# Kernel tuning notes

Hardware: AMD Instinct MI355X
Metric: run time of the kernel (lower is better)

The kernel has to match this reference:

```python
import jax, jax.numpy as jnp
import numpy as np

N = 50000      # nodes per graph
G = 5          # num_graphs
F = 128        # in_channels
E0 = 800000    # random edges (avg degree 16)
H1, C1 = 8, 8  # conv1: heads=8, out=8 -> concat 64
C2 = 16        # conv2: heads=1, out=out_channels
NEG_SLOPE = 0.2


def setup_inputs() -> dict:
    key = jax.random.key(0)
    ks = jax.random.split(key, 12)
    x = jax.random.normal(ks[0], (G, N, F), dtype=jnp.float32)
    er = jax.random.randint(ks[1], (G, 2, E0), 0, N, dtype=jnp.int32)
    loops = jnp.broadcast_to(jnp.arange(N, dtype=jnp.int32), (G, 2, N))
    edge_index = jnp.concatenate([er, loops], axis=-1)  # [G, 2, E0+N] with self loops
    s = 0.1
    W1 = jax.random.normal(ks[2], (F, H1 * C1), jnp.float32) * s
    a_src1 = jax.random.normal(ks[3], (H1, C1), jnp.float32) * s
    a_dst1 = jax.random.normal(ks[4], (H1, C1), jnp.float32) * s
    b1 = jnp.zeros((H1 * C1,), jnp.float32)
    W2 = jax.random.normal(ks[5], (H1 * C1, C2), jnp.float32) * s
    a_src2 = jax.random.normal(ks[6], (1, C2), jnp.float32) * s
    a_dst2 = jax.random.normal(ks[7], (1, C2), jnp.float32) * s
    b2 = jnp.zeros((C2,), jnp.float32)
    Wf = jax.random.normal(ks[8], (C2 * G, 2), jnp.float32) * s
    bf = jnp.zeros((2,), jnp.float32)
    return {"x": x, "edge_index": edge_index, "W1": W1, "a_src1": a_src1,
            "a_dst1": a_dst1, "b1": b1, "W2": W2, "a_src2": a_src2,
            "a_dst2": a_dst2, "b2": b2, "Wf": Wf, "bf": bf}


def gat_layer(x, src, dst, W, a_src, a_dst, b):
    # x: [N, Fin]; src/dst: [E]; W: [Fin, H*C]; a_src/a_dst: [H, C]; b: [H*C]
    H, C = a_src.shape
    h = (x @ W).reshape(-1, H, C)                       # [N, H, C]
    alpha_s = jnp.einsum('nhc,hc->nh', h, a_src)        # [N, H]
    alpha_d = jnp.einsum('nhc,hc->nh', h, a_dst)
    e = jax.nn.leaky_relu(alpha_s[src] + alpha_d[dst], NEG_SLOPE)  # [E, H]
    m = jax.ops.segment_max(e, dst, num_segments=N)     # per-target softmax (stable)
    ex = jnp.exp(e - m[dst])
    denom = jax.ops.segment_sum(ex, dst, num_segments=N)
    alpha = ex / (denom[dst] + 1e-16)                   # [E, H]
    out = jax.ops.segment_sum(alpha[:, :, None] * h[src], dst, num_segments=N)  # [N, H, C]
    return out.reshape(-1, H * C) + b


def reference(x, edge_index, W1, a_src1, a_dst1, b1, W2, a_src2, a_dst2, b2, Wf, bf):
    def per_graph(xg, eg):
        src, dst = eg[0], eg[1]  # messages flow source -> target (PyG convention)
        h = jax.nn.relu(gat_layer(xg, src, dst, W1, a_src1, a_dst1, b1))
        return gat_layer(h, src, dst, W2, a_src2, a_dst2, b2)  # [N, C2]
    x_seq = jax.vmap(per_graph)(x, edge_index)          # [G, N, C2]
    x_seq = jnp.transpose(x_seq, (1, 0, 2)).reshape(N, G * C2)
    return x_seq @ Wf + bf                               # [N, 2]
```

## Files before the change

### kernel.cpp

```cpp
#include <hip/hip_runtime.h>

constexpr int N_NODES = 50000;
constexpr int G = 5;
constexpr int E = 850000;
constexpr int GN = G * N_NODES;
constexpr int GE = G * E;
constexpr float SLOPE = 0.2f;

constexpr int NPB = 1024;
constexpr int NBUK = (GN + NPB - 1) / NPB;
constexpr int EPB = 4096;
constexpr int NBLK_E = (GE + EPB - 1) / EPB;

static __device__ __forceinline__ float lrelu(float e) {
    return e > 0.f ? e : SLOPE * e;
}
static __device__ __forceinline__ unsigned short f2h(float f) {
    union { _Float16 h; unsigned short u; } v;
    v.h = (_Float16)f;
    return v.u;
}
static __device__ __forceinline__ float h2f(unsigned short u) {
    union { unsigned short u; _Float16 h; } v;
    v.u = u;
    return (float)v.h;
}

__global__ __launch_bounds__(256) void k_hist(const int* __restrict__ ei,
                                              int* __restrict__ H) {
    __shared__ int hist[NBUK];
    const int t = threadIdx.x, bi = blockIdx.x;
    for (int j = t; j < NBUK; j += 256) hist[j] = 0;
    __syncthreads();
#pragma unroll
    for (int i = 0; i < 16; ++i) {
        int idx = bi * EPB + i * 256 + t;
        if (idx < GE) {
            int g = idx / E;
            int el = idx - g * E;
            int dst = ei[(size_t)g * 2 * E + E + el];
            atomicAdd(&hist[(g * N_NODES + dst) >> 10], 1);
        }
    }
    __syncthreads();
    for (int j = t; j < NBUK; j += 256) H[(size_t)bi * NBUK + j] = hist[j];
}

__global__ __launch_bounds__(256) void k_scanH(int* __restrict__ H,
                                               int* __restrict__ T) {
    __shared__ int s[256];
    const int t = threadIdx.x, b = blockIdx.x;
    int run = 0;
    for (int c = 0; c < NBLK_E; c += 256) {
        int bi = c + t;
        int v = (bi < NBLK_E) ? H[(size_t)bi * NBUK + b] : 0;
        s[t] = v;
        for (int off = 1; off < 256; off <<= 1) {
            __syncthreads();
            int u = (t >= off) ? s[t - off] : 0;
            __syncthreads();
            s[t] += u;
        }
        __syncthreads();
        int excl = s[t] - v;
        if (bi < NBLK_E) H[(size_t)bi * NBUK + b] = run + excl;
        run += s[255];
        __syncthreads();
    }
    if (t == 0) T[b] = run;
}

__global__ __launch_bounds__(256) void k_scanT(const int* __restrict__ T,
                                               int* __restrict__ base_g) {
    __shared__ int s[256];
    const int t = threadIdx.x;
    int v = (t < NBUK) ? T[t] : 0;
    s[t] = v;
    for (int off = 1; off < 256; off <<= 1) {
        __syncthreads();
        int u = (t >= off) ? s[t - off] : 0;
        __syncthreads();
        s[t] += u;
    }
    __syncthreads();
    if (t < NBUK) base_g[t] = s[t] - v;
    if (t == 0) base_g[NBUK] = s[255];
}

__global__ __launch_bounds__(256) void k_scatter(const int* __restrict__ ei,
                                                 const int* __restrict__ H,
                                                 const int* __restrict__ base_g,
                                                 int* __restrict__ tmp) {
    __shared__ int cnt[NBUK];
    __shared__ int off[NBUK];
    const int t = threadIdx.x, bi = blockIdx.x;
    for (int j = t; j < NBUK; j += 256) {
        cnt[j] = 0;
        off[j] = base_g[j] + H[(size_t)bi * NBUK + j];
    }
    __syncthreads();
#pragma unroll
    for (int i = 0; i < 16; ++i) {
        int idx = bi * EPB + i * 256 + t;
        if (idx < GE) {
            int g = idx / E;
            int el = idx - g * E;
            const int* eb = ei + (size_t)g * 2 * E;
            int src = eb[el];
            int dst = eb[E + el];
            int gdst = g * N_NODES + dst;
            int b = gdst >> 10;
            int rank = atomicAdd(&cnt[b], 1);
            tmp[off[b] + rank] = ((gdst & 1023) << 18) | (g * N_NODES + src);
        }
    }
}

__global__ __launch_bounds__(256) void k_build(const int* __restrict__ base_g,
                                               const int* __restrict__ tmp,
                                               int* __restrict__ rowptr,
                                               int* __restrict__ deg,
                                               int* __restrict__ csr) {
    __shared__ int degL[NPB];
    __shared__ int curL[NPB];
    __shared__ int s[256];
    const int t = threadIdx.x, b = blockIdx.x;
    const int n0 = b << 10;
    const int nn = min(NPB, GN - n0);
    const int s0 = base_g[b], s1 = base_g[b + 1];
#pragma unroll
    for (int i = 0; i < 4; ++i) degL[t * 4 + i] = 0;
    __syncthreads();
    for (int i = s0 + t; i < s1; i += 256)
        atomicAdd(&degL[tmp[i] >> 18], 1);
    __syncthreads();
    int j0 = t * 4;
    int d0 = degL[j0], d1 = degL[j0 + 1], d2 = degL[j0 + 2], d3 = degL[j0 + 3];
    int tsum = d0 + d1 + d2 + d3;
    s[t] = tsum;
    for (int off = 1; off < 256; off <<= 1) {
        __syncthreads();
        int u = (t >= off) ? s[t - off] : 0;
        __syncthreads();
        s[t] += u;
    }
    __syncthreads();
    int excl = s[t] - tsum;
    int p0 = excl, p1 = p0 + d0, p2 = p1 + d1, p3 = p2 + d2;
    curL[j0] = p0; curL[j0 + 1] = p1; curL[j0 + 2] = p2; curL[j0 + 3] = p3;
    if (j0     < nn) { rowptr[n0 + j0]     = s0 + p0; deg[n0 + j0]     = d0; }
    if (j0 + 1 < nn) { rowptr[n0 + j0 + 1] = s0 + p1; deg[n0 + j0 + 1] = d1; }
    if (j0 + 2 < nn) { rowptr[n0 + j0 + 2] = s0 + p2; deg[n0 + j0 + 2] = d2; }
    if (j0 + 3 < nn) { rowptr[n0 + j0 + 3] = s0 + p3; deg[n0 + j0 + 3] = d3; }
    __syncthreads();
    for (int i = s0 + t; i < s1; i += 256) {
        int e = tmp[i];
        int r = atomicAdd(&curL[e >> 18], 1);
        csr[s0 + r] = e & 0x3FFFF;
    }
}

__global__ __launch_bounds__(256) void k_gemm1(const float* __restrict__ x,
                                               const float* __restrict__ W1,
                                               const float* __restrict__ a_src,
                                               const float* __restrict__ a_dst,
                                               unsigned short* __restrict__ h1f,
                                               unsigned short* __restrict__ l1,
                                               float* __restrict__ ad1) {
    __shared__ float Bs[128][68];
    __shared__ float As[64][65];
    __shared__ float aS[64], aD[64];
    const int t = threadIdx.x;
    const int rowBase = blockIdx.x * 64;

    const float4* W14 = (const float4*)W1;
#pragma unroll
    for (int i = 0; i < 8; ++i) {
        int v = t + i * 256;
        int k = v >> 4;
        int c = (v & 15) << 2;
        float4 w = W14[v];
        Bs[k][c] = w.x; Bs[k][c + 1] = w.y; Bs[k][c + 2] = w.z; Bs[k][c + 3] = w.w;
    }
    if (t < 64) { aS[t] = a_src[t]; aD[t] = a_dst[t]; }

    const int tx = t & 15;
    const int ty = t >> 4;
    float acc[4][4] = {};
    const float4* x4 = (const float4*)x;

    for (int kc = 0; kc < 128; kc += 64) {
        __syncthreads();
#pragma unroll
        for (int i = 0; i < 4; ++i) {
            int v = t + i * 256;
            int r = v >> 4;
            int kq = v & 15;
            int row = rowBase + r;
            float4 a = make_float4(0.f, 0.f, 0.f, 0.f);
            if (row < GN) a = x4[row * 32 + (kc >> 2) + kq];
            int kk = kq << 2;
            As[kk][r] = a.x; As[kk + 1][r] = a.y; As[kk + 2][r] = a.z; As[kk + 3][r] = a.w;
        }
        __syncthreads();
#pragma unroll 8
        for (int k = 0; k < 64; ++k) {
            float a0 = As[k][ty * 4 + 0];
            float a1 = As[k][ty * 4 + 1];
            float a2 = As[k][ty * 4 + 2];
            float a3 = As[k][ty * 4 + 3];
            float4 b = *(const float4*)&Bs[kc + k][tx * 4];
            acc[0][0] += a0 * b.x; acc[0][1] += a0 * b.y; acc[0][2] += a0 * b.z; acc[0][3] += a0 * b.w;
            acc[1][0] += a1 * b.x; acc[1][1] += a1 * b.y; acc[1][2] += a1 * b.z; acc[1][3] += a1 * b.w;
            acc[2][0] += a2 * b.x; acc[2][1] += a2 * b.y; acc[2][2] += a2 * b.z; acc[2][3] += a2 * b.w;
            acc[3][0] += a3 * b.x; acc[3][1] += a3 * b.y; acc[3][2] += a3 * b.z; acc[3][3] += a3 * b.w;
        }
    }
    const int head = tx >> 1;
    const int coff = (tx & 1) * 4;
#pragma unroll
    for (int i = 0; i < 4; ++i) {
        int row = rowBase + ty * 4 + i;
        float as_p = acc[i][0] * aS[head * 8 + coff]     + acc[i][1] * aS[head * 8 + coff + 1]
                   + acc[i][2] * aS[head * 8 + coff + 2] + acc[i][3] * aS[head * 8 + coff + 3];
        float ad_p = acc[i][0] * aD[head * 8 + coff]     + acc[i][1] * aD[head * 8 + coff + 1]
                   + acc[i][2] * aD[head * 8 + coff + 2] + acc[i][3] * aD[head * 8 + coff + 3];
        as_p += __shfl_xor(as_p, 1);
        ad_p += __shfl_xor(ad_p, 1);
        if (row < GN) {
            ushort4 fv = make_ushort4(f2h(acc[i][0]), f2h(acc[i][1]), f2h(acc[i][2]), f2h(acc[i][3]));
            *(ushort4*)(h1f + (size_t)row * 64 + tx * 4) = fv;
            if ((tx & 1) == 0) {
                l1[(size_t)row * 8 + head] = f2h(as_p);
                ad1[row * 8 + head] = ad_p;
            }
        }
    }
}

__global__ __launch_bounds__(256) void k_layer1(const int* __restrict__ rowptr,
                                                const int* __restrict__ deg,
                                                const int* __restrict__ csr,
                                                const unsigned short* __restrict__ h1f,
                                                const unsigned short* __restrict__ l1,
                                                const float* __restrict__ ad1,
                                                unsigned short* __restrict__ out1h) {
    int d = __builtin_amdgcn_readfirstlane(blockIdx.x * 4 + (threadIdx.x >> 6));
    int tt = threadIdx.x & 63;
    int half = tt >> 5;
    int p = tt & 31;
    int h = p >> 2;
    int start = rowptr[d];
    int dg = deg[d];
    float ad = ad1[d * 8 + h];
    const unsigned int* h1d = (const unsigned int*)h1f;
    float den = 0.f, accx = 0.f, accy = 0.f;
    int j = 0;
    for (; j + 8 <= dg; j += 8) {
        int s[4];
#pragma unroll
        for (int e = 0; e < 4; ++e) {
            int se = csr[start + j + 2 * e];
            int so = csr[start + j + 2 * e + 1];
            s[e] = half ? so : se;
        }
        float w[4];
#pragma unroll
        for (int e = 0; e < 4; ++e)
            w[e] = __expf(lrelu(h2f(l1[(size_t)s[e] * 8 + h]) + ad));
        unsigned int gp[4];
#pragma unroll
        for (int e = 0; e < 4; ++e) gp[e] = h1d[(size_t)s[e] * 32 + p];
#pragma unroll
        for (int e = 0; e < 4; ++e) {
            den += w[e];
            accx += w[e] * h2f((unsigned short)(gp[e] & 0xffff));
            accy += w[e] * h2f((unsigned short)(gp[e] >> 16));
        }
    }
    for (; j < dg; j += 2) {
        int se = csr[start + j];
        int so = (j + 1 < dg) ? csr[start + j + 1] : se;
        int s = half ? so : se;
        float w = __expf(lrelu(h2f(l1[(size_t)s * 8 + h]) + ad));
        if (j + half >= dg) w = 0.f;
        unsigned int gp = h1d[(size_t)s * 32 + p];
        den += w;
        accx += w * h2f((unsigned short)(gp & 0xffff));
        accy += w * h2f((unsigned short)(gp >> 16));
    }
    accx += __shfl_xor(accx, 32);
    accy += __shfl_xor(accy, 32);
    den  += __shfl_xor(den, 32);
    if (half == 0) {
        float inv = 1.f / (den + 1e-16f);
        unsigned int pk = (unsigned int)f2h(accx * inv)
                        | ((unsigned int)f2h(accy * inv) << 16);
        ((unsigned int*)out1h)[(size_t)d * 32 + p] = pk;
    }
}

__global__ __launch_bounds__(256) void k_gemm2(const unsigned short* __restrict__ agg1,
                                               const float* __restrict__ b1,
                                               const float* __restrict__ W2,
                                               const float* __restrict__ a_src,
                                               const float* __restrict__ a_dst,
                                               unsigned short* __restrict__ h2r,
                                               float* __restrict__ ad2) {
    __shared__ float As[64][65];
    __shared__ float Bs[64][20];
    __shared__ float aS[16], aD[16];
    const int t = threadIdx.x;
    const int rowBase = blockIdx.x * 64;

    {
        int k = t >> 2, c = (t & 3) << 2;
        float4 w = ((const float4*)W2)[t];
        Bs[k][c] = w.x; Bs[k][c + 1] = w.y; Bs[k][c + 2] = w.z; Bs[k][c + 3] = w.w;
    }
    if (t < 16) { aS[t] = a_src[t]; aD[t] = a_dst[t]; }
    const ushort4* a4p = (const ushort4*)agg1;
    const float4* b14 = (const float4*)b1;
#pragma unroll
    for (int i = 0; i < 4; ++i) {
        int v = t + i * 256;
        int r = v >> 4;
        int kq = v & 15;
        int row = rowBase + r;
        float ax = 0.f, ay = 0.f, az = 0.f, aw = 0.f;
        if (row < GN) {
            ushort4 a = a4p[row * 16 + kq];
            float4 bb = b14[kq];
            ax = fmaxf(h2f(a.x) + bb.x, 0.f);
            ay = fmaxf(h2f(a.y) + bb.y, 0.f);
            az = fmaxf(h2f(a.z) + bb.z, 0.f);
            aw = fmaxf(h2f(a.w) + bb.w, 0.f);
        }
        int kk = kq << 2;
        As[kk][r] = ax; As[kk + 1][r] = ay; As[kk + 2][r] = az; As[kk + 3][r] = aw;
    }
    __syncthreads();
    const int r = t >> 2;
    const int cg = (t & 3) << 2;
    float acc0 = 0.f, acc1 = 0.f, acc2 = 0.f, acc3 = 0.f;
#pragma unroll 8
    for (int k = 0; k < 64; ++k) {
        float a = As[k][r];
        float4 b = *(const float4*)&Bs[k][cg];
        acc0 += a * b.x; acc1 += a * b.y; acc2 += a * b.z; acc3 += a * b.w;
    }
    float as_p = acc0 * aS[cg] + acc1 * aS[cg + 1] + acc2 * aS[cg + 2] + acc3 * aS[cg + 3];
    float ad_p = acc0 * aD[cg] + acc1 * aD[cg + 1] + acc2 * aD[cg + 2] + acc3 * aD[cg + 3];
    as_p += __shfl_xor(as_p, 1); as_p += __shfl_xor(as_p, 2);
    ad_p += __shfl_xor(ad_p, 1); ad_p += __shfl_xor(ad_p, 2);
    int row = rowBase + r;
    if (row < GN) {
        ushort4 fv = make_ushort4(f2h(acc0), f2h(acc1), f2h(acc2), f2h(acc3));
        *(ushort4*)(h2r + (size_t)row * 20 + cg) = fv;
        if ((t & 3) == 0) {
            h2r[(size_t)row * 20 + 16] = f2h(as_p);
            ad2[row] = ad_p;
        }
    }
}

__global__ __launch_bounds__(256) void k_layer2(const int* __restrict__ rowptr,
                                                const int* __restrict__ deg,
                                                const int* __restrict__ csr,
                                                const unsigned short* __restrict__ h2r,
                                                const float* __restrict__ ad2,
                                                float* __restrict__ out2) {
    int d = __builtin_amdgcn_readfirstlane(blockIdx.x * 4 + (threadIdx.x >> 6));
    int tt = threadIdx.x & 63;
    int p = tt & 7;
    int sub = tt >> 3;
    int start = rowptr[d];
    int dg = deg[d];
    float ad = ad2[d];
    int sv = csr[start + min(tt, dg - 1)];
    int full = min(dg, 64);
    float den = 0.f, accx = 0.f, accy = 0.f;
    for (int base = 0; base < full; base += 8) {
        int j = base + sub;
        bool val = j < full;
        int s = __shfl(sv, j < 64 ? j : 0);
        const unsigned short* r = h2r + (size_t)s * 20;
        float w = val ? __expf(lrelu(h2f(r[16]) + ad)) : 0.f;
        unsigned int gp = *(const unsigned int*)(r + p * 2);
        den += w;
        accx += w * h2f((unsigned short)(gp & 0xffff));
        accy += w * h2f((unsigned short)(gp >> 16));
    }
    for (int base = 64; base < dg; base += 8) {
        int j = base + sub;
        bool val = j < dg;
        int s = csr[start + (val ? j : 0)];
        const unsigned short* r = h2r + (size_t)s * 20;
        float w = val ? __expf(lrelu(h2f(r[16]) + ad)) : 0.f;
        unsigned int gp = *(const unsigned int*)(r + p * 2);
        den += w;
        accx += w * h2f((unsigned short)(gp & 0xffff));
        accy += w * h2f((unsigned short)(gp >> 16));
    }
    accx += __shfl_xor(accx, 8); accx += __shfl_xor(accx, 16); accx += __shfl_xor(accx, 32);
    accy += __shfl_xor(accy, 8); accy += __shfl_xor(accy, 16); accy += __shfl_xor(accy, 32);
    den  += __shfl_xor(den, 8);  den  += __shfl_xor(den, 16);  den  += __shfl_xor(den, 32);
    if (sub == 0) {
        float inv = 1.f / (den + 1e-16f);
        ((float2*)out2)[(size_t)d * 8 + p] = make_float2(accx * inv, accy * inv);
    }
}

__global__ __launch_bounds__(256) void k_final(const float* __restrict__ agg2,
                                               const float* __restrict__ b2,
                                               const float* __restrict__ Wf,
                                               const float* __restrict__ bf,
                                               float* __restrict__ out) {
    int n = blockIdx.x * 256 + threadIdx.x;
    if (n >= N_NODES) return;
    float o0 = bf[0], o1 = bf[1];
#pragma unroll
    for (int g = 0; g < G; ++g) {
        const float4* v4 = (const float4*)agg2 + (size_t)(g * N_NODES + n) * 4;
#pragma unroll
        for (int q = 0; q < 4; ++q) {
            float4 v = v4[q];
            float4 b = ((const float4*)b2)[q];
            v.x += b.x; v.y += b.y; v.z += b.z; v.w += b.w;
            int kb = g * 16 + q * 4;
            o0 += v.x * Wf[(kb + 0) * 2]     + v.y * Wf[(kb + 1) * 2]
                + v.z * Wf[(kb + 2) * 2]     + v.w * Wf[(kb + 3) * 2];
            o1 += v.x * Wf[(kb + 0) * 2 + 1] + v.y * Wf[(kb + 1) * 2 + 1]
                + v.z * Wf[(kb + 2) * 2 + 1] + v.w * Wf[(kb + 3) * 2 + 1];
        }
    }
    out[n * 2]     = o0;
    out[n * 2 + 1] = o1;
}

extern "C" void kernel_launch(void* const* d_in, const int* in_sizes, int n_in,
                              void* d_out, int out_size, void* d_ws, size_t ws_size,
                              hipStream_t stream) {
    const float* x      = (const float*)d_in[0];
    const int*   ei     = (const int*)d_in[1];
    const float* W1     = (const float*)d_in[2];
    const float* a_src1 = (const float*)d_in[3];
    const float* a_dst1 = (const float*)d_in[4];
    const float* b1     = (const float*)d_in[5];
    const float* W2     = (const float*)d_in[6];
    const float* a_src2 = (const float*)d_in[7];
    const float* a_dst2 = (const float*)d_in[8];
    const float* b2     = (const float*)d_in[9];
    const float* Wf     = (const float*)d_in[10];
    const float* bf     = (const float*)d_in[11];
    float* out = (float*)d_out;

    unsigned short* h1f = (unsigned short*)d_ws;
    unsigned short* l1  = h1f + (size_t)GN * 64;
    unsigned short* h2r = h1f;
    float* out2 = (float*)(h2r + (size_t)GN * 20);
    unsigned short* out1h = h1f + (size_t)GN * 72;
    float* ad1  = (float*)(out1h + (size_t)GN * 64);
    float* ad2  = ad1;
    int*   iws    = (int*)(ad1 + (size_t)GN * 8);
    int*   rowptr = iws;
    int*   deg    = rowptr + GN;
    int*   base_g = deg + GN;
    int*   T      = base_g + (NBUK + 1);
    int*   H      = T + NBUK;
    int*   tmp    = H + (size_t)NBLK_E * NBUK;
    int*   csr    = tmp + GE;

    k_hist   <<<NBLK_E, 256, 0, stream>>>(ei, H);
    k_scanH  <<<NBUK,   256, 0, stream>>>(H, T);
    k_scanT  <<<1,      256, 0, stream>>>(T, base_g);
    k_scatter<<<NBLK_E, 256, 0, stream>>>(ei, H, base_g, tmp);
    k_build  <<<NBUK,   256, 0, stream>>>(base_g, tmp, rowptr, deg, csr);

    k_gemm1  <<<(GN + 63) / 64, 256, 0, stream>>>(x, W1, a_src1, a_dst1, h1f, l1, ad1);
    k_layer1 <<<GN / 4, 256, 0, stream>>>(rowptr, deg, csr, h1f, l1, ad1, out1h);
    k_gemm2  <<<(GN + 63) / 64, 256, 0, stream>>>(out1h, b1, W2, a_src2, a_dst2, h2r, ad2);
    k_layer2 <<<GN / 4, 256, 0, stream>>>(rowptr, deg, csr, h2r, ad2, out2);
    k_final  <<<(N_NODES + 255) / 256, 256, 0, stream>>>(out2, b2, Wf, bf, out);
}
```

Before: 567.5 us.

## Remap layer-1 aggregation to 32 lanes per node with 16-byte gathers

The layer-1 aggregation kernel now gives each destination node 32 lanes instead of 64. Each lane handles one head with 8 channels, loaded as one uint4, and takes every fourth edge; partial sums are combined with xor shuffles across the 4 edge slots. This cuts the number of per-edge exp and attention-logit loads per channel and uses wider vector gathers and stores, with twice as many nodes per block. In exchange, the per-node loop is no longer unrolled, so fewer independent loads are in flight per lane, and the final reduction needs extra shuffles.

```diff
diff --git a/kernel.cpp b/kernel.cpp
--- a/kernel.cpp
+++ b/kernel.cpp
@@ -245,58 +245,51 @@
                                                 const unsigned short* __restrict__ l1,
                                                 const float* __restrict__ ad1,
                                                 unsigned short* __restrict__ out1h) {
-    int d = __builtin_amdgcn_readfirstlane(blockIdx.x * 4 + (threadIdx.x >> 6));
-    int tt = threadIdx.x & 63;
-    int half = tt >> 5;
-    int p = tt & 31;
-    int h = p >> 2;
-    int start = rowptr[d];
-    int dg = deg[d];
-    float ad = ad1[d * 8 + h];
+    const int tt = threadIdx.x & 63;
+    const int h  = tt & 7;
+    const int es = (tt >> 3) & 3;
+    const int d  = blockIdx.x * 8 + (threadIdx.x >> 5);
+
+    const int start = rowptr[d];
+    const int dg    = deg[d];
+    const float ad  = ad1[d * 8 + h];
+
     const unsigned int* h1d = (const unsigned int*)h1f;
-    float den = 0.f, accx = 0.f, accy = 0.f;
-    int j = 0;
-    for (; j + 8 <= dg; j += 8) {
-        int s[4];
-#pragma unroll
-        for (int e = 0; e < 4; ++e) {
-            int se = csr[start + j + 2 * e];
-            int so = csr[start + j + 2 * e + 1];
-            s[e] = half ? so : se;
-        }
-        float w[4];
-#pragma unroll
-        for (int e = 0; e < 4; ++e)
-            w[e] = __expf(lrelu(h2f(l1[(size_t)s[e] * 8 + h]) + ad));
-        unsigned int gp[4];
-#pragma unroll
-        for (int e = 0; e < 4; ++e) gp[e] = h1d[(size_t)s[e] * 32 + p];
-#pragma unroll
-        for (int e = 0; e < 4; ++e) {
-            den += w[e];
-            accx += w[e] * h2f((unsigned short)(gp[e] & 0xffff));
-            accy += w[e] * h2f((unsigned short)(gp[e] >> 16));
-        }
-    }
-    for (; j < dg; j += 2) {
-        int se = csr[start + j];
-        int so = (j + 1 < dg) ? csr[start + j + 1] : se;
-        int s = half ? so : se;
+    float a0 = 0.f, a1 = 0.f, a2 = 0.f, a3 = 0.f;
+    float a4 = 0.f, a5 = 0.f, a6 = 0.f, a7 = 0.f;
+    float den = 0.f;
+
+    for (int j = es; j < dg; j += 4) {
+        int s = csr[start + j];
         float w = __expf(lrelu(h2f(l1[(size_t)s * 8 + h]) + ad));
-        if (j + half >= dg) w = 0.f;
-        unsigned int gp = h1d[(size_t)s * 32 + p];
         den += w;
-        accx += w * h2f((unsigned short)(gp & 0xffff));
-        accy += w * h2f((unsigned short)(gp >> 16));
-    }
-    accx += __shfl_xor(accx, 32);
-    accy += __shfl_xor(accy, 32);
-    den  += __shfl_xor(den, 32);
-    if (half == 0) {
+        const uint4 gp = *(const uint4*)(h1d + (size_t)s * 32 + h * 4);
+        a0 += w * h2f((unsigned short)(gp.x & 0xffff));
+        a1 += w * h2f((unsigned short)(gp.x >> 16));
+        a2 += w * h2f((unsigned short)(gp.y & 0xffff));
+        a3 += w * h2f((unsigned short)(gp.y >> 16));
+        a4 += w * h2f((unsigned short)(gp.z & 0xffff));
+        a5 += w * h2f((unsigned short)(gp.z >> 16));
+        a6 += w * h2f((unsigned short)(gp.w & 0xffff));
+        a7 += w * h2f((unsigned short)(gp.w >> 16));
+    }
+    a0 += __shfl_xor(a0, 8);  a0 += __shfl_xor(a0, 16);
+    a1 += __shfl_xor(a1, 8);  a1 += __shfl_xor(a1, 16);
+    a2 += __shfl_xor(a2, 8);  a2 += __shfl_xor(a2, 16);
+    a3 += __shfl_xor(a3, 8);  a3 += __shfl_xor(a3, 16);
+    a4 += __shfl_xor(a4, 8);  a4 += __shfl_xor(a4, 16);
+    a5 += __shfl_xor(a5, 8);  a5 += __shfl_xor(a5, 16);
+    a6 += __shfl_xor(a6, 8);  a6 += __shfl_xor(a6, 16);
+    a7 += __shfl_xor(a7, 8);  a7 += __shfl_xor(a7, 16);
+    den += __shfl_xor(den, 8); den += __shfl_xor(den, 16);
+
+    if (es == 0) {
         float inv = 1.f / (den + 1e-16f);
-        unsigned int pk = (unsigned int)f2h(accx * inv)
-                        | ((unsigned int)f2h(accy * inv) << 16);
-        ((unsigned int*)out1h)[(size_t)d * 32 + p] = pk;
+        unsigned int p0 = (unsigned int)f2h(a0 * inv) | ((unsigned int)f2h(a1 * inv) << 16);
+        unsigned int p1 = (unsigned int)f2h(a2 * inv) | ((unsigned int)f2h(a3 * inv) << 16);
+        unsigned int p2 = (unsigned int)f2h(a4 * inv) | ((unsigned int)f2h(a5 * inv) << 16);
+        unsigned int p3 = (unsigned int)f2h(a6 * inv) | ((unsigned int)f2h(a7 * inv) << 16);
+        *(uint4*)(out1h + (size_t)d * 64 + h * 8) = make_uint4(p0, p1, p2, p3);
     }
 }
 
@@ -478,7 +471,7 @@
     k_build  <<<NBUK,   256, 0, stream>>>(base_g, tmp, rowptr, deg, csr);
 
     k_gemm1  <<<(GN + 63) / 64, 256, 0, stream>>>(x, W1, a_src1, a_dst1, h1f, l1, ad1);
-    k_layer1 <<<GN / 4, 256, 0, stream>>>(rowptr, deg, csr, h1f, l1, ad1, out1h);
+    k_layer1 <<<GN / 8, 256, 0, stream>>>(rowptr, deg, csr, h1f, l1, ad1, out1h);
     k_gemm2  <<<(GN + 63) / 64, 256, 0, stream>>>(out1h, b1, W2, a_src2, a_dst2, h2r, ad2);
     k_layer2 <<<GN / 4, 256, 0, stream>>>(rowptr, deg, csr, h2r, ad2, out2);
     k_final  <<<(N_NODES + 255) / 256, 256, 0, stream>>>(out2, b2, Wf, bf, out);
```

After: 550.6 us. 3.0% less time.
